# Performance work log

Measured on AMD Instinct MI355X. Metric: run time of the kernel, lower is better.

## Reference

```python
import jax, jax.numpy as jnp
import numpy as np

N_EMBD = 1024
N_HEAD = 16

def _lin_params(key, fan_in, fan_out):
    kw, kb = jax.random.split(key)
    bound = 1.0 / np.sqrt(fan_in)
    W = jax.random.uniform(kw, (fan_in, fan_out), minval=-bound, maxval=bound, dtype=jnp.float32)
    b = jax.random.uniform(kb, (fan_out,), minval=-bound, maxval=bound, dtype=jnp.float32)
    return W, b

def setup_inputs() -> dict:
    key = jax.random.key(0)
    ks = jax.random.split(key, 6)
    x = jax.random.normal(ks[0], (2, 2048, N_EMBD), dtype=jnp.float32)
    W_attn, b_attn = _lin_params(ks[1], N_EMBD, 3 * N_EMBD)
    W_proj, b_proj = _lin_params(ks[2], N_EMBD, N_EMBD)
    W_fc, b_fc = _lin_params(ks[3], N_EMBD, 4 * N_EMBD)
    W_fc2, b_fc2 = _lin_params(ks[4], 4 * N_EMBD, N_EMBD)
    ln1_g = jnp.ones((N_EMBD,), jnp.float32); ln1_b = jnp.zeros((N_EMBD,), jnp.float32)
    ln2_g = jnp.ones((N_EMBD,), jnp.float32); ln2_b = jnp.zeros((N_EMBD,), jnp.float32)
    return {"x": x, "W_attn": W_attn, "b_attn": b_attn, "W_proj": W_proj, "b_proj": b_proj,
            "W_fc": W_fc, "b_fc": b_fc, "W_fc2": W_fc2, "b_fc2": b_fc2,
            "ln1_g": ln1_g, "ln1_b": ln1_b, "ln2_g": ln2_g, "ln2_b": ln2_b}

def _layernorm(x, g, b, eps=1e-5):
    mu = jnp.mean(x, axis=-1, keepdims=True)
    var = jnp.var(x, axis=-1, keepdims=True)
    return (x - mu) * jax.lax.rsqrt(var + eps) * g + b

def _attention(x, W_attn, b_attn, W_proj, b_proj):
    B, T, C = x.shape
    hd = C // N_HEAD
    qkv = x @ W_attn + b_attn                      # [B,T,3C]
    q, k, v = jnp.split(qkv, 3, axis=-1)
    # [B,T,C] -> [B,H,T,hd]
    q = q.reshape(B, T, N_HEAD, hd).transpose(0, 2, 1, 3)
    k = k.reshape(B, T, N_HEAD, hd).transpose(0, 2, 1, 3)
    v = v.reshape(B, T, N_HEAD, hd).transpose(0, 2, 1, 3)
    att = jnp.einsum('bhqd,bhkd->bhqk', q, k) * (1.0 / np.sqrt(hd))
    causal = jnp.tril(jnp.ones((T, T), bool))
    att = jnp.where(causal[None, None], att, -jnp.inf)
    att = jax.nn.softmax(att, axis=-1)
    y = jnp.einsum('bhqk,bhkd->bhqd', att, v)      # [B,H,T,hd]
    y = y.transpose(0, 2, 1, 3).reshape(B, T, C)
    return y @ W_proj + b_proj

def _mlp(x, W_fc, b_fc, W_fc2, b_fc2):
    h = jax.nn.gelu(x @ W_fc + b_fc, approximate=False)
    return h @ W_fc2 + b_fc2

def reference(x, W_attn, b_attn, W_proj, b_proj, W_fc, b_fc, W_fc2, b_fc2,
              ln1_g, ln1_b, ln2_g, ln2_b):
    x = x + _attention(_layernorm(x, ln1_g, ln1_b), W_attn, b_attn, W_proj, b_proj)
    x = x + _mlp(_layernorm(x, ln2_g, ln2_b), W_fc, b_fc, W_fc2, b_fc2)
    return x
```

## Files before the change

### kernel.cpp

```cpp
#include <hip/hip_runtime.h>
#include <cstdint>
#include <cstddef>


typedef unsigned short u16;
typedef short bf16x8 __attribute__((ext_vector_type(8)));
typedef float f32x4 __attribute__((ext_vector_type(4)));

#define C_EMBD 1024
#define T_SEQ  2048
#define N_BATCH 2
#define N_HEADS 16
#define HEAD_D 64
#define M_TOK  4096
#define Q_SCALE 0.18033688011112042f

__device__ __forceinline__ u16 f2b(float f) {
  union { float f; unsigned u; } v; v.f = f;
  unsigned r = (v.u + 0x7fffu + ((v.u >> 16) & 1u)) >> 16;
  return (u16)r;
}
__device__ __forceinline__ float b2f(u16 u) {
  union { unsigned u; float f; } v; v.u = ((unsigned)u) << 16;
  return v.f;
}
__device__ __forceinline__ unsigned pk2(float a, float b) {
  union { float f; unsigned u; } x, y; x.f = a; y.f = b;
  return __builtin_amdgcn_perm(y.u, x.u, 0x07060302u);
}
__device__ __forceinline__ void load_lds16(const void* g, void* l) {
  __builtin_amdgcn_global_load_lds(
      (const __attribute__((address_space(1))) void*)g,
      (__attribute__((address_space(3))) void*)l, 16, 0, 0);
}
__device__ __forceinline__ float gelu_fast(float x) {
  const float p = x * __builtin_fmaf(0.044715f * x, x, 1.0f);
  const float t = __builtin_amdgcn_exp2f(2.3021859215f * p);
  return x * t * __builtin_amdgcn_rcpf(t + 1.0f);
}

__global__ __launch_bounds__(256) void transpose_cast(
    const float* __restrict__ W, u16* __restrict__ Wt, int K, int N) {
  __shared__ float tile[32][33];
  const int n0 = blockIdx.x * 32, k0 = blockIdx.y * 32;
  const int tx = threadIdx.x & 31, ty = threadIdx.x >> 5;
#pragma unroll
  for (int i = 0; i < 32; i += 8)
    tile[ty + i][tx] = W[(size_t)(k0 + ty + i) * N + n0 + tx];
  __syncthreads();
#pragma unroll
  for (int i = 0; i < 32; i += 8)
    Wt[(size_t)(n0 + ty + i) * K + k0 + tx] = f2b(tile[tx][ty + i]);
}

__global__ __launch_bounds__(256) void ln_cast(
    const float* __restrict__ X, const float* __restrict__ g,
    const float* __restrict__ b, u16* __restrict__ Y) {
  const int row = blockIdx.x;
  const int tid = threadIdx.x;
  const float4 v = ((const float4*)(X + (size_t)row * C_EMBD))[tid];
  float s = v.x + v.y + v.z + v.w;
  float ss = v.x * v.x + v.y * v.y + v.z * v.z + v.w * v.w;
#pragma unroll
  for (int off = 32; off > 0; off >>= 1) {
    s += __shfl_down(s, off, 64);
    ss += __shfl_down(ss, off, 64);
  }
  __shared__ float red[8];
  __shared__ float stats[2];
  const int wave = tid >> 6, lane = tid & 63;
  if (lane == 0) { red[wave] = s; red[4 + wave] = ss; }
  __syncthreads();
  if (tid == 0) {
    float S = red[0] + red[1] + red[2] + red[3];
    float SS = red[4] + red[5] + red[6] + red[7];
    float mu = S * (1.0f / C_EMBD);
    float var = SS * (1.0f / C_EMBD) - mu * mu;
    stats[0] = mu;
    stats[1] = rsqrtf(var + 1e-5f);
  }
  __syncthreads();
  const float mu = stats[0], rs = stats[1];
  const float4 gv = ((const float4*)g)[tid];
  const float4 bv = ((const float4*)b)[tid];
  ushort4 o;
  o.x = f2b((v.x - mu) * rs * gv.x + bv.x);
  o.y = f2b((v.y - mu) * rs * gv.y + bv.y);
  o.z = f2b((v.z - mu) * rs * gv.z + bv.z);
  o.w = f2b((v.w - mu) * rs * gv.w + bv.w);
  ((ushort4*)(Y + (size_t)row * C_EMBD))[tid] = o;
}

__global__ __launch_bounds__(256) void ln_reduce_cast(
    const float* __restrict__ P0, const float* __restrict__ P1,
    const float* __restrict__ bias, const float* __restrict__ res,
    const float* __restrict__ g, const float* __restrict__ b,
    float* __restrict__ X1, u16* __restrict__ Y) {
  const int row = blockIdx.x;
  const int tid = threadIdx.x;
  const size_t base = (size_t)row * C_EMBD;
  const float4 p0 = ((const float4*)(P0 + base))[tid];
  const float4 p1 = ((const float4*)(P1 + base))[tid];
  const float4 rr = ((const float4*)(res + base))[tid];
  const float4 bb = ((const float4*)bias)[tid];
  float4 v;
  v.x = p0.x + p1.x + rr.x + bb.x;
  v.y = p0.y + p1.y + rr.y + bb.y;
  v.z = p0.z + p1.z + rr.z + bb.z;
  v.w = p0.w + p1.w + rr.w + bb.w;
  ((float4*)(X1 + base))[tid] = v;
  float s = v.x + v.y + v.z + v.w;
  float ss = v.x * v.x + v.y * v.y + v.z * v.z + v.w * v.w;
#pragma unroll
  for (int off = 32; off > 0; off >>= 1) {
    s += __shfl_down(s, off, 64);
    ss += __shfl_down(ss, off, 64);
  }
  __shared__ float red[8];
  __shared__ float stats[2];
  const int wave = tid >> 6, lane = tid & 63;
  if (lane == 0) { red[wave] = s; red[4 + wave] = ss; }
  __syncthreads();
  if (tid == 0) {
    float S = red[0] + red[1] + red[2] + red[3];
    float SS = red[4] + red[5] + red[6] + red[7];
    float mu = S * (1.0f / C_EMBD);
    float var = SS * (1.0f / C_EMBD) - mu * mu;
    stats[0] = mu;
    stats[1] = rsqrtf(var + 1e-5f);
  }
  __syncthreads();
  const float mu = stats[0], rs = stats[1];
  const float4 gv = ((const float4*)g)[tid];
  const float4 bv = ((const float4*)b)[tid];
  ushort4 o;
  o.x = f2b((v.x - mu) * rs * gv.x + bv.x);
  o.y = f2b((v.y - mu) * rs * gv.y + bv.y);
  o.z = f2b((v.z - mu) * rs * gv.z + bv.z);
  o.w = f2b((v.w - mu) * rs * gv.w + bv.w);
  ((ushort4*)(Y + base))[tid] = o;
}

enum { EPI_BF16 = 0, EPI_GELU_BF16 = 2, EPI_PART = 3, EPI_QKV = 4 };

template <int EPI, int SPLIT>
__global__ __launch_bounds__(256) void gemm_bt(
    const u16* __restrict__ A, const u16* __restrict__ Bt,
    const float* __restrict__ bias,
    void* __restrict__ Cout, void* __restrict__ Cout2, void* __restrict__ Cout3,
    int M, int N, int K) {
  __shared__ u16 As[128 * 64];
  __shared__ u16 Bs[128 * 64];
  const int tid = threadIdx.x;
  const int wave = tid >> 6, lane = tid & 63;
  const int quad = lane >> 4, l16 = lane & 15;
  const int sw = l16 & 7;

  const int nBx = (int)gridDim.x;
  const int id = (int)blockIdx.y * nBx + (int)blockIdx.x;
  const int span = 8 * nBx;
  const int gid = id / span, rem = id % span;
  const int mt = gid * 8 + (rem & 7), nt_ = rem >> 3;
  const int m0 = mt * 128, n0 = nt_ * 128;

  const int wm = (wave >> 1) * 64, wn = (wave & 1) * 64;

  f32x4 acc[4][4] = {};

  const int kTiles = (K >> 6) / SPLIT;
  const int kt0 = (SPLIT == 2) ? (int)blockIdx.z * kTiles : 0;
  for (int kt = kt0; kt < kt0 + kTiles; ++kt) {
    const int k0 = kt << 6;
#pragma unroll
    for (int i = 0; i < 4; ++i) {
      const int c = tid + i * 256;
      const int row = c >> 3, gc = ((c & 7) ^ (row & 7)) * 8;
      load_lds16(A + (size_t)(m0 + row) * K + k0 + gc, &As[c * 8]);
    }
#pragma unroll
    for (int i = 0; i < 4; ++i) {
      const int c = tid + i * 256;
      const int row = c >> 3, gc = ((c & 7) ^ (row & 7)) * 8;
      load_lds16(Bt + (size_t)(n0 + row) * K + k0 + gc, &Bs[c * 8]);
    }
    __syncthreads();
#pragma unroll
    for (int ks = 0; ks < 2; ++ks) {
      bf16x8 aF[4], bF[4];
#pragma unroll
      for (int t = 0; t < 4; ++t) {
        aF[t] = *(const bf16x8*)
            &As[(wm + t * 16 + l16) * 64 + (((ks * 4 + quad) ^ sw) * 8)];
        bF[t] = *(const bf16x8*)
            &Bs[(wn + t * 16 + l16) * 64 + (((ks * 4 + quad) ^ sw) * 8)];
      }
#pragma unroll
      for (int tm = 0; tm < 4; ++tm)
#pragma unroll
        for (int tn = 0; tn < 4; ++tn)
          acc[tm][tn] = __builtin_amdgcn_mfma_f32_16x16x32_bf16(
              bF[tn], aF[tm], acc[tm][tn], 0, 0, 0);
    }
    __syncthreads();
  }

  float* Pz = (float*)((SPLIT == 2 && blockIdx.z == 1) ? Cout2 : Cout);
#pragma unroll
  for (int tm = 0; tm < 4; ++tm) {
    const int row = m0 + wm + tm * 16 + l16;
#pragma unroll
    for (int tn = 0; tn < 4; ++tn) {
      const int col = n0 + wn + tn * 16 + quad * 4;
      if constexpr (EPI == EPI_PART) {
        *(float4*)&Pz[(size_t)row * N + col] = *(float4*)&acc[tm][tn];
      } else if constexpr (EPI == EPI_QKV) {
        const int bb = row >> 11, t = row & (T_SEQ - 1);
        const float4 bz = *(const float4*)&bias[col];
        float v0 = acc[tm][tn][0] + bz.x, v1 = acc[tm][tn][1] + bz.y;
        float v2 = acc[tm][tn][2] + bz.z, v3 = acc[tm][tn][3] + bz.w;
        const int sec = col >> 10;
        const int h = (col & 1023) >> 6, d4 = col & 63;
        const int bh = bb * N_HEADS + h;
        if (sec == 0) {
          ushort4 o;
          o.x = f2b(v0 * Q_SCALE); o.y = f2b(v1 * Q_SCALE);
          o.z = f2b(v2 * Q_SCALE); o.w = f2b(v3 * Q_SCALE);
          *(ushort4*)&((u16*)Cout)[((size_t)bh * T_SEQ + t) * HEAD_D + d4] = o;
        } else if (sec == 1) {
          ushort4 o;
          o.x = f2b(v0); o.y = f2b(v1); o.z = f2b(v2); o.w = f2b(v3);
          *(ushort4*)&((u16*)Cout2)[((size_t)bh * T_SEQ + t) * HEAD_D + d4] = o;
        } else {
          u16* vp = (u16*)Cout3 + ((size_t)bh * HEAD_D + d4) * T_SEQ + t;
          vp[0] = f2b(v0); vp[T_SEQ] = f2b(v1);
          vp[2 * T_SEQ] = f2b(v2); vp[3 * T_SEQ] = f2b(v3);
        }
      } else {
        const float4 bz = *(const float4*)&bias[col];
        float v0 = acc[tm][tn][0] + bz.x, v1 = acc[tm][tn][1] + bz.y;
        float v2 = acc[tm][tn][2] + bz.z, v3 = acc[tm][tn][3] + bz.w;
        if constexpr (EPI == EPI_GELU_BF16) {
          v0 = gelu_fast(v0); v1 = gelu_fast(v1);
          v2 = gelu_fast(v2); v3 = gelu_fast(v3);
        }
        ushort4 o;
        o.x = f2b(v0); o.y = f2b(v1); o.z = f2b(v2); o.w = f2b(v3);
        *(ushort4*)&((u16*)Cout)[(size_t)row * N + col] = o;
      }
    }
  }
}

__global__ __launch_bounds__(256) void reduce_add(
    const float* __restrict__ P0, const float* __restrict__ P1,
    const float* __restrict__ bias, const float* __restrict__ res,
    float* __restrict__ out) {
  const int idx = blockIdx.x * 256 + threadIdx.x;
  const float4 a = ((const float4*)P0)[idx];
  const float4 b = ((const float4*)P1)[idx];
  const float4 c = ((const float4*)res)[idx];
  const float4 g = ((const float4*)bias)[idx & 255];
  float4 o;
  o.x = a.x + b.x + c.x + g.x;
  o.y = a.y + b.y + c.y + g.y;
  o.z = a.z + b.z + c.z + g.z;
  o.w = a.w + b.w + c.w + g.w;
  ((float4*)out)[idx] = o;
}

__global__ __launch_bounds__(256) void attn_fwd(
    const u16* __restrict__ Q, const u16* __restrict__ Kb,
    const u16* __restrict__ Vt, u16* __restrict__ Y) {
  const int bh = blockIdx.y;
  const int pair = blockIdx.x;
  const int nqt = (int)(T_SEQ / 64);
  const int tid = threadIdx.x;
  const int wave = tid >> 6, lane = tid & 63;
  const int quad = lane >> 4, l16 = lane & 15;
  const int sw = l16 & 7;
  const u16* Qp = Q + (size_t)bh * T_SEQ * HEAD_D;
  const u16* Kp = Kb + (size_t)bh * T_SEQ * HEAD_D;
  const u16* Vp = Vt + (size_t)bh * HEAD_D * T_SEQ;

  __shared__ u16 Ks[2][64 * 64];
  __shared__ u16 Vs[2][64 * 64];
  __shared__ u16 Pl[4][16 * 72];

  const int c1 = tid, c2 = tid + 256;
  const int r1 = c1 >> 3, g1 = ((c1 & 7) ^ (r1 & 7)) * 8;
  const int r2 = c2 >> 3, g2 = ((c2 & 7) ^ (r2 & 7)) * 8;
  const size_t kO1 = (size_t)r1 * HEAD_D + g1, kO2 = (size_t)r2 * HEAD_D + g2;
  const size_t vO1 = (size_t)r1 * T_SEQ + g1, vO2 = (size_t)r2 * T_SEQ + g2;
  u16* const dK1[2] = {&Ks[0][c1 * 8], &Ks[1][c1 * 8]};
  u16* const dK2[2] = {&Ks[0][c2 * 8], &Ks[1][c2 * 8]};
  u16* const dV1[2] = {&Vs[0][c1 * 8], &Vs[1][c1 * 8]};
  u16* const dV2[2] = {&Vs[0][c2 * 8], &Vs[1][c2 * 8]};

  auto stageK = [&](int bb, int k0) {
    const u16* base = Kp + (size_t)k0 * HEAD_D;
    load_lds16(base + kO1, dK1[bb]);
    load_lds16(base + kO2, dK2[bb]);
  };
  auto stageV = [&](int bb, int k0) {
    const u16* base = Vp + k0;
    load_lds16(base + vO1, dV1[bb]);
    load_lds16(base + vO2, dV2[bb]);
  };

  const int b = bh >> 4, h = bh & 15;

#pragma unroll 1
  for (int phase = 0; phase < 2; ++phase) {
    const int qb = phase == 0 ? (nqt - 1 - pair) : pair;
    const int q0 = qb * 64;
    const int qglob = q0 + wave * 16 + l16;

    if (phase == 1) __syncthreads();

    bf16x8 qF[2];
    qF[0] = *(const bf16x8*)&Qp[(size_t)qglob * HEAD_D + quad * 8];
    qF[1] = *(const bf16x8*)&Qp[(size_t)qglob * HEAD_D + 32 + quad * 8];

    f32x4 o[4] = {};
    float mrun = -3e38f, lrun = 0.0f;

    stageK(0, 0);
    stageV(0, 0);

    int buf = 0;
    for (int kb = 0; kb <= qb; ++kb) {
      const int k0 = kb * 64;
      __syncthreads();
      if (kb < qb) {
        stageK(buf ^ 1, k0 + 64);
        stageV(buf ^ 1, k0 + 64);
      }
      f32x4 st[4] = {};
#pragma unroll
      for (int ks = 0; ks < 2; ++ks) {
#pragma unroll
        for (int nt = 0; nt < 4; ++nt) {
          bf16x8 kF = *(const bf16x8*)
              &Ks[buf][(nt * 16 + l16) * 64 + (((ks * 4 + quad) ^ sw) * 8)];
          st[nt] = __builtin_amdgcn_mfma_f32_16x16x32_bf16(kF, qF[ks], st[nt],
                                                           0, 0, 0);
        }
      }
      if (kb == qb) {
#pragma unroll
        for (int nt = 0; nt < 4; ++nt) {
#pragma unroll
          for (int r = 0; r < 4; ++r) {
            const int key = k0 + nt * 16 + quad * 4 + r;
            if (key > qglob) st[nt][r] = -3e38f;
          }
        }
      }
      float m = st[0][0];
#pragma unroll
      for (int nt = 0; nt < 4; ++nt)
#pragma unroll
        for (int r = 0; r < 4; ++r) m = fmaxf(m, st[nt][r]);
      m = fmaxf(m, __shfl_xor(m, 16, 64));
      m = fmaxf(m, __shfl_xor(m, 32, 64));
      const float nm = fmaxf(mrun, m);
      const float alpha = __builtin_amdgcn_exp2f(mrun - nm);
      mrun = nm;
      float sum = 0.0f;
#pragma unroll
      for (int nt = 0; nt < 4; ++nt)
#pragma unroll
        for (int r = 0; r < 4; ++r) {
          const float p = __builtin_amdgcn_exp2f(st[nt][r] - nm);
          st[nt][r] = p;
          sum += p;
        }
      sum += __shfl_xor(sum, 16, 64);
      sum += __shfl_xor(sum, 32, 64);
      lrun = lrun * alpha + sum;
#pragma unroll
      for (int nt = 0; nt < 4; ++nt)
#pragma unroll
        for (int r = 0; r < 4; ++r) o[nt][r] *= alpha;
#pragma unroll
      for (int nt = 0; nt < 4; ++nt) {
        uint2 pk;
        pk.x = pk2(st[nt][0], st[nt][1]);
        pk.y = pk2(st[nt][2], st[nt][3]);
        *(uint2*)&Pl[wave][l16 * 72 + nt * 16 + quad * 4] = pk;
      }
#pragma unroll
      for (int ks = 0; ks < 2; ++ks) {
        bf16x8 aP = *(const bf16x8*)&Pl[wave][l16 * 72 + ks * 32 + quad * 8];
#pragma unroll
        for (int nt = 0; nt < 4; ++nt) {
          bf16x8 vF = *(const bf16x8*)
              &Vs[buf][(nt * 16 + l16) * 64 + (((ks * 4 + quad) ^ sw) * 8)];
          o[nt] =
              __builtin_amdgcn_mfma_f32_16x16x32_bf16(vF, aP, o[nt], 0, 0, 0);
        }
      }
      buf ^= 1;
    }

    const float rl = 1.0f / lrun;
    u16* yp = Y + ((size_t)(b * T_SEQ + qglob)) * C_EMBD + h * HEAD_D;
#pragma unroll
    for (int nt = 0; nt < 4; ++nt) {
      ushort4 ov;
      ov.x = f2b(o[nt][0] * rl); ov.y = f2b(o[nt][1] * rl);
      ov.z = f2b(o[nt][2] * rl); ov.w = f2b(o[nt][3] * rl);
      *(ushort4*)&yp[nt * 16 + quad * 4] = ov;
    }
  }
}

extern "C" void kernel_launch(void* const* d_in, const int* in_sizes, int n_in,
                              void* d_out, int out_size, void* d_ws,
                              size_t ws_size, hipStream_t stream) {
  const float* x      = (const float*)d_in[0];
  const float* W_attn = (const float*)d_in[1];
  const float* b_attn = (const float*)d_in[2];
  const float* W_proj = (const float*)d_in[3];
  const float* b_proj = (const float*)d_in[4];
  const float* W_fc   = (const float*)d_in[5];
  const float* b_fc   = (const float*)d_in[6];
  const float* W_fc2  = (const float*)d_in[7];
  const float* b_fc2  = (const float*)d_in[8];
  const float* ln1_g  = (const float*)d_in[9];
  const float* ln1_b  = (const float*)d_in[10];
  const float* ln2_g  = (const float*)d_in[11];
  const float* ln2_b  = (const float*)d_in[12];

  u16* wqkvT = (u16*)d_ws;
  u16* wprojT = wqkvT + (size_t)3072 * 1024;
  u16* wfcT  = wprojT + (size_t)1024 * 1024;
  u16* wfc2T = wfcT + (size_t)4096 * 1024;
  u16* Abuf  = wfc2T + (size_t)1024 * 4096;
  float* x1  = (float*)(Abuf + (size_t)M_TOK * C_EMBD);
  u16* hbuf  = (u16*)(x1 + (size_t)M_TOK * C_EMBD);
  float* projP = (float*)hbuf;
  u16* Qb    = hbuf + (size_t)M_TOK * 4096;
  u16* Kbuf  = Qb + (size_t)32 * T_SEQ * HEAD_D;
  u16* Vtb   = Kbuf + (size_t)32 * T_SEQ * HEAD_D;
  float* fc2P1 = (float*)Qb;

  const dim3 blk(256);

  transpose_cast<<<dim3(3072 / 32, 1024 / 32), blk, 0, stream>>>(W_attn, wqkvT, 1024, 3072);
  transpose_cast<<<dim3(1024 / 32, 1024 / 32), blk, 0, stream>>>(W_proj, wprojT, 1024, 1024);
  transpose_cast<<<dim3(4096 / 32, 1024 / 32), blk, 0, stream>>>(W_fc, wfcT, 1024, 4096);
  transpose_cast<<<dim3(1024 / 32, 4096 / 32), blk, 0, stream>>>(W_fc2, wfc2T, 4096, 1024);

  ln_cast<<<M_TOK, blk, 0, stream>>>(x, ln1_g, ln1_b, Abuf);

  gemm_bt<EPI_QKV, 1><<<dim3(3072 / 128, M_TOK / 128), blk, 0, stream>>>(
      Abuf, wqkvT, b_attn, Qb, Kbuf, Vtb, M_TOK, 3072, 1024);

  attn_fwd<<<dim3(T_SEQ / 128, 32), blk, 0, stream>>>(Qb, Kbuf, Vtb, Abuf);

  gemm_bt<EPI_PART, 2><<<dim3(1024 / 128, M_TOK / 128, 2), blk, 0, stream>>>(
      Abuf, wprojT, nullptr, projP, projP + (size_t)M_TOK * C_EMBD, nullptr,
      M_TOK, 1024, 1024);
  ln_reduce_cast<<<M_TOK, blk, 0, stream>>>(
      projP, projP + (size_t)M_TOK * C_EMBD, b_proj, x, ln2_g, ln2_b,
      x1, Abuf);

  gemm_bt<EPI_GELU_BF16, 1><<<dim3(4096 / 128, M_TOK / 128), blk, 0, stream>>>(
      Abuf, wfcT, b_fc, hbuf, nullptr, nullptr, M_TOK, 4096, 1024);

  gemm_bt<EPI_PART, 2><<<dim3(1024 / 128, M_TOK / 128, 2), blk, 0, stream>>>(
      hbuf, wfc2T, nullptr, d_out, fc2P1, nullptr, M_TOK, 1024, 4096);
  reduce_add<<<M_TOK * C_EMBD / 1024, blk, 0, stream>>>(
      (const float*)d_out, fc2P1, b_fc2, x1, (float*)d_out);
}
```

Baseline: 353.8 us.

## Merge weight transposes into one launch, remap GEMM and attention block order

The four weight transpose-cast launches become a single kernel that picks its matrix from the block index, saving launch overhead and tail gaps. The GEMM block-to-tile mapping switches to a fixed scheme that groups 32 M-tiles per N column, and attention blocks are reordered so consecutive blocks cover different heads. GEMM global and LDS offsets are now computed once outside the K loop. The hardcoded GEMM mapping assumes exactly 32 M-tiles (M=4096) and ignores gridDim.z, which fits the current shapes but would silently break for others.

```diff
diff --git a/kernel.cpp b/kernel.cpp
--- a/kernel.cpp
+++ b/kernel.cpp
@@ -39,10 +39,20 @@
   return x * t * __builtin_amdgcn_rcpf(t + 1.0f);
 }
 
-__global__ __launch_bounds__(256) void transpose_cast(
-    const float* __restrict__ W, u16* __restrict__ Wt, int K, int N) {
+__global__ __launch_bounds__(256) void transpose_cast_all(
+    const float* __restrict__ W0, u16* __restrict__ D0,
+    const float* __restrict__ W1, u16* __restrict__ D1,
+    const float* __restrict__ W2, u16* __restrict__ D2,
+    const float* __restrict__ W3, u16* __restrict__ D3) {
+  int id = blockIdx.x;
+  const float* W; u16* D; int K, N, t;
+  if (id < 3072)      { W = W0; D = D0; K = 1024; N = 3072; t = id; }
+  else if (id < 4096) { W = W1; D = D1; K = 1024; N = 1024; t = id - 3072; }
+  else if (id < 8192) { W = W2; D = D2; K = 1024; N = 4096; t = id - 4096; }
+  else                { W = W3; D = D3; K = 4096; N = 1024; t = id - 8192; }
+  const int nTN = N >> 5;
+  const int n0 = (t % nTN) * 32, k0 = (t / nTN) * 32;
   __shared__ float tile[32][33];
-  const int n0 = blockIdx.x * 32, k0 = blockIdx.y * 32;
   const int tx = threadIdx.x & 31, ty = threadIdx.x >> 5;
 #pragma unroll
   for (int i = 0; i < 32; i += 8)
@@ -50,7 +60,7 @@
   __syncthreads();
 #pragma unroll
   for (int i = 0; i < 32; i += 8)
-    Wt[(size_t)(n0 + ty + i) * K + k0 + tx] = f2b(tile[tx][ty + i]);
+    D[(size_t)(n0 + ty + i) * K + k0 + tx] = f2b(tile[tx][ty + i]);
 }
 
 __global__ __launch_bounds__(256) void ln_cast(
@@ -156,33 +166,36 @@
   const int quad = lane >> 4, l16 = lane & 15;
   const int sw = l16 & 7;
 
-  const int nBx = (int)gridDim.x;
-  const int id = (int)blockIdx.y * nBx + (int)blockIdx.x;
-  const int span = 8 * nBx;
-  const int gid = id / span, rem = id % span;
-  const int mt = gid * 8 + (rem & 7), nt_ = rem >> 3;
+  const int id = (int)blockIdx.y * (int)gridDim.x + (int)blockIdx.x;
+  const int mt = ((id & 7) << 2) + ((id >> 3) & 3);
+  const int nt_ = id >> 5;
   const int m0 = mt * 128, n0 = nt_ * 128;
 
   const int wm = (wave >> 1) * 64, wn = (wave & 1) * 64;
 
   f32x4 acc[4][4] = {};
+
+  size_t aOff[4], bOff[4];
+  int ldsOff[4];
+#pragma unroll
+  for (int i = 0; i < 4; ++i) {
+    const int c = tid + i * 256;
+    const int row = c >> 3, gc = ((c & 7) ^ (row & 7)) * 8;
+    aOff[i] = (size_t)(m0 + row) * K + gc;
+    bOff[i] = (size_t)(n0 + row) * K + gc;
+    ldsOff[i] = c * 8;
+  }
 
   const int kTiles = (K >> 6) / SPLIT;
   const int kt0 = (SPLIT == 2) ? (int)blockIdx.z * kTiles : 0;
   for (int kt = kt0; kt < kt0 + kTiles; ++kt) {
     const int k0 = kt << 6;
 #pragma unroll
-    for (int i = 0; i < 4; ++i) {
-      const int c = tid + i * 256;
-      const int row = c >> 3, gc = ((c & 7) ^ (row & 7)) * 8;
-      load_lds16(A + (size_t)(m0 + row) * K + k0 + gc, &As[c * 8]);
-    }
-#pragma unroll
-    for (int i = 0; i < 4; ++i) {
-      const int c = tid + i * 256;
-      const int row = c >> 3, gc = ((c & 7) ^ (row & 7)) * 8;
-      load_lds16(Bt + (size_t)(n0 + row) * K + k0 + gc, &Bs[c * 8]);
-    }
+    for (int i = 0; i < 4; ++i)
+      load_lds16(A + aOff[i] + k0, &As[ldsOff[i]]);
+#pragma unroll
+    for (int i = 0; i < 4; ++i)
+      load_lds16(Bt + bOff[i] + k0, &Bs[ldsOff[i]]);
     __syncthreads();
 #pragma unroll
     for (int ks = 0; ks < 2; ++ks) {
@@ -271,8 +284,9 @@
 __global__ __launch_bounds__(256) void attn_fwd(
     const u16* __restrict__ Q, const u16* __restrict__ Kb,
     const u16* __restrict__ Vt, u16* __restrict__ Y) {
-  const int bh = blockIdx.y;
-  const int pair = blockIdx.x;
+  const int id = (int)blockIdx.y * (int)gridDim.x + (int)blockIdx.x;
+  const int bh = (id & 7) + (((id >> 3) & 3) << 3);
+  const int pair = id >> 5;
   const int nqt = (int)(T_SEQ / 64);
   const int tid = threadIdx.x;
   const int wave = tid >> 6, lane = tid & 63;
@@ -447,10 +461,8 @@
 
   const dim3 blk(256);
 
-  transpose_cast<<<dim3(3072 / 32, 1024 / 32), blk, 0, stream>>>(W_attn, wqkvT, 1024, 3072);
-  transpose_cast<<<dim3(1024 / 32, 1024 / 32), blk, 0, stream>>>(W_proj, wprojT, 1024, 1024);
-  transpose_cast<<<dim3(4096 / 32, 1024 / 32), blk, 0, stream>>>(W_fc, wfcT, 1024, 4096);
-  transpose_cast<<<dim3(1024 / 32, 4096 / 32), blk, 0, stream>>>(W_fc2, wfc2T, 4096, 1024);
+  transpose_cast_all<<<12288, blk, 0, stream>>>(
+      W_attn, wqkvT, W_proj, wprojT, W_fc, wfcT, W_fc2, wfc2T);
 
   ln_cast<<<M_TOK, blk, 0, stream>>>(x, ln1_g, ln1_b, Abuf);
 
```

Measured after the change: 330.7 us. 1.07x faster.
